# Kernel optimization log

Hardware: AMD Instinct MI355X
Metric: run time of the kernel (lower is better)

Reference implementation:

```python
import jax, jax.numpy as jnp
import numpy as np

PIECES = 64  # self.plane


def _proj(f, w1, b1, w2, b2):
    # Projection: fc2(relu(fc1(f))), final_relu=False
    h = jax.nn.relu(f @ w1 + b1)
    return h @ w2 + b2


def _cf(img, param, pieces):
    # img: [B,3,H,W], param: [B,3,P]
    # total[b,c,h,w] = sum_i clamp(img - i/P, 0, 1/P) * param[b,c,i], then * P / sum_i param
    grid = jnp.arange(pieces, dtype=img.dtype) / pieces            # [P]
    clipped = jnp.clip(img[..., None] - grid, 0.0, 1.0 / pieces)   # [B,3,H,W,P]
    total = jnp.einsum('bchwp,bcp->bchw', clipped, param)
    norm = pieces / (jnp.sum(param, axis=-1) + 1e-30)              # [B,3]
    return total * norm[:, :, None, None]


def setup_inputs() -> dict:
    key = jax.random.key(0)
    ks = jax.random.split(key, 11)
    B, H, W = 8, 256, 256
    s = 0.05
    return {
        'x': jax.random.uniform(ks[0], (B, 3, H, W), jnp.float32),
        'f_feature': jax.random.normal(ks[1], (B, 512), jnp.float32),
        'b_feature': jax.random.normal(ks[2], (B, 512), jnp.float32),
        # stacked weights for [fc_f_1, fc_b_1, fc_f_s, fc_b_s]
        'proj_w1': jax.random.normal(ks[3], (4, 512, 192), jnp.float32) * s,
        'proj_b1': jax.random.normal(ks[4], (4, 192), jnp.float32) * s,
        'proj_w2': jax.random.normal(ks[5], (4, 192, 192), jnp.float32) * s,
        'proj_b2': jax.random.normal(ks[6], (4, 192), jnp.float32) * s,
        'fc_w1': jax.random.normal(ks[7], (576, 192), jnp.float32) * s,
        'fc_b1': jax.random.normal(ks[8], (192,), jnp.float32) * s,
        'fc_w2': jax.random.normal(ks[9], (192, 192), jnp.float32) * s,
        'fc_b2': jax.random.normal(ks[10], (192,), jnp.float32) * s,
    }


def reference(x, f_feature, b_feature, proj_w1, proj_b1, proj_w2, proj_b2,
              fc_w1, fc_b1, fc_w2, fc_b2):
    B = x.shape[0]
    # rgb_to_grayscale with 3 output channels (ITU-R 601 weights)
    gw = jnp.array([0.299, 0.587, 0.114], dtype=x.dtype)
    gray = jnp.broadcast_to(jnp.einsum('bchw,c->bhw', x, gw)[:, None], x.shape)

    # four stacked Projections: inputs [f, b, f, b]
    feats = jnp.stack([f_feature, b_feature, f_feature, b_feature])       # [4,B,512]
    h = jax.nn.relu(jnp.einsum('kbi,kio->kbo', feats, proj_w1) + proj_b1[:, None, :])
    outs = jnp.einsum('kbo,koq->kbq', h, proj_w2) + proj_b2[:, None, :]   # [4,B,192]
    param_f, param_b = outs[0], outs[1]
    param_s = outs[2] + outs[3]

    cat = jnp.concatenate([param_f, param_b, param_s], axis=1)            # [B,576]
    param = _proj(cat, fc_w1, fc_b1, fc_w2, fc_b2)                        # [B,192]

    p_all = param.reshape(B, 3, PIECES)
    p_f = param_f.reshape(B, 3, PIECES)
    p_b = param_b.reshape(B, 3, PIECES)

    return (_cf(x, p_all, PIECES), _cf(gray, p_f, PIECES), _cf(gray, p_b, PIECES))
```

## Files before the change

### kernel.cpp

```cpp
#include <hip/hip_runtime.h>

#define HWSZ 65536
#define PLANE (3 * HWSZ)
#define OUTSTRIDE (8 * PLANE)
#define MAGIC 0x13572468

__global__ __launch_bounds__(384) void k_mlp(
    const float* __restrict__ f, const float* __restrict__ bf,
    const float* __restrict__ pw1, const float* __restrict__ pb1,
    const float* __restrict__ pw2, const float* __restrict__ pb2,
    const float* __restrict__ fw1, const float* __restrict__ fb1,
    const float* __restrict__ fw2, const float* __restrict__ fb2,
    float* __restrict__ ws) {
  __shared__ float smem[2304];
  int t = threadIdx.x, blk = blockIdx.x;

  float* pA      = ws;
  float* partial = ws + 12288;
  int* fbase = (int*)(ws + 20480);

  int s = blk & 7, b = blk >> 3;
  int k = s >> 1, half = s & 1, o0 = half * 96;
  {
    float* sf  = smem;
    float* red = smem + 512;
    float* sh  = smem + 2048;

    const float* feat = ((k & 1) ? bf : f) + b * 512;
    for (int i = t; i < 512; i += 384) sf[i] = feat[i];
    __syncthreads();

    {
      int q = t % 24, sr = t / 24;
      const float4* w = (const float4*)(pw1 + (size_t)k * (512 * 192));
      int icol = half * 24 + q;
      float4 acc = {0.f, 0.f, 0.f, 0.f};
      int i0 = sr * 32;
      for (int r = 0; r < 2; ++r) {
        float4 wv[16];
#pragma unroll
        for (int j = 0; j < 16; ++j)
          wv[j] = w[(size_t)(i0 + r * 16 + j) * 48 + icol];
#pragma unroll
        for (int j = 0; j < 16; ++j) {
          float v = sf[i0 + r * 16 + j];
          acc.x = fmaf(v, wv[j].x, acc.x); acc.y = fmaf(v, wv[j].y, acc.y);
          acc.z = fmaf(v, wv[j].z, acc.z); acc.w = fmaf(v, wv[j].w, acc.w);
        }
      }
      ((float4*)(red + sr * 96))[q] = acc;
    }
    __syncthreads();
    if (t < 96) {
      float a = pb1[k * 192 + o0 + t];
#pragma unroll
      for (int s2 = 0; s2 < 16; ++s2) a += red[s2 * 96 + t];
      sh[t] = fmaxf(a, 0.f);
    }
    __syncthreads();
    {
      int q2 = t % 48, s2 = t / 48;
      const float4* w = (const float4*)(pw2 + (size_t)k * (192 * 192));
      float4 acc = {0.f, 0.f, 0.f, 0.f};
      float4 wv[12];
#pragma unroll
      for (int j = 0; j < 12; ++j)
        wv[j] = w[(size_t)(o0 + s2 * 12 + j) * 48 + q2];
#pragma unroll
      for (int j = 0; j < 12; ++j) {
        float v = sh[s2 * 12 + j];
        acc.x = fmaf(v, wv[j].x, acc.x); acc.y = fmaf(v, wv[j].y, acc.y);
        acc.z = fmaf(v, wv[j].z, acc.z); acc.w = fmaf(v, wv[j].w, acc.w);
      }
      ((float4*)(red + s2 * 192))[q2] = acc;
    }
    __syncthreads();
    if (t < 192) {
      float a = 0.f;
#pragma unroll
      for (int s3 = 0; s3 < 8; ++s3) a += red[s3 * 192 + t];
      pA[((k * 8 + b) * 2 + half) * 192 + t] = a;
    }
    __syncthreads();
    if (t == 0) {
      __threadfence();
      atomicExch(&fbase[blk * 16], MAGIC);
    }
  }

  if (s >= 4) return;

  int b2 = b, c4 = s, ob2 = c4 * 48;
  int q = t % 12, sb = t / 12;
  int q2 = t % 48, s2 = t / 48;

  float4 wv1[18];
  {
    const float4* w = (const float4*)fw1;
    int i0 = sb * 18;
#pragma unroll
    for (int j = 0; j < 18; ++j)
      wv1[j] = w[(size_t)(i0 + j) * 48 + c4 * 12 + q];
  }
  float4 wv2[6];
  {
    const float4* w = (const float4*)fw2;
#pragma unroll
    for (int j = 0; j < 6; ++j)
      wv2[j] = w[(size_t)(ob2 + s2 * 6 + j) * 48 + q2];
  }

  if (t < 8) {
    while (atomicAdd(&fbase[((b2 << 3) + t) * 16], 0) != MAGIC)
      __builtin_amdgcn_s_sleep(2);
  }
  __syncthreads();
  if (t == 0) __threadfence();
  __syncthreads();

  {
    float* sc  = smem;
    float* red = smem + 576;
    for (int idx = t; idx < 576; idx += 384) {
      float v;
      if (idx < 192) {
        const float* p0 = pA + ((0 * 8 + b2) * 2) * 192;
        v = p0[idx] + p0[192 + idx] + pb2[idx];
      } else if (idx < 384) {
        int jj = idx - 192;
        const float* p1 = pA + ((1 * 8 + b2) * 2) * 192;
        v = p1[jj] + p1[192 + jj] + pb2[192 + jj];
      } else {
        int jj = idx - 384;
        const float* p2 = pA + ((2 * 8 + b2) * 2) * 192;
        const float* p3 = pA + ((3 * 8 + b2) * 2) * 192;
        v = p2[jj] + p2[192 + jj] + p3[jj] + p3[192 + jj] +
            pb2[384 + jj] + pb2[576 + jj];
      }
      sc[idx] = v;
    }
    __syncthreads();
    {
      float4 acc = {0.f, 0.f, 0.f, 0.f};
      int i0 = sb * 18;
#pragma unroll
      for (int j = 0; j < 18; ++j) {
        float v = sc[i0 + j];
        acc.x = fmaf(v, wv1[j].x, acc.x); acc.y = fmaf(v, wv1[j].y, acc.y);
        acc.z = fmaf(v, wv1[j].z, acc.z); acc.w = fmaf(v, wv1[j].w, acc.w);
      }
      ((float4*)(red + sb * 48))[q] = acc;
    }
    __syncthreads();
    if (t < 48) {
      float a = fb1[ob2 + t];
#pragma unroll
      for (int s3 = 0; s3 < 32; ++s3) a += red[s3 * 48 + t];
      smem[t] = fmaxf(a, 0.f);
    }
    __syncthreads();
    {
      float4 acc = {0.f, 0.f, 0.f, 0.f};
#pragma unroll
      for (int j = 0; j < 6; ++j) {
        float v = smem[s2 * 6 + j];
        acc.x = fmaf(v, wv2[j].x, acc.x); acc.y = fmaf(v, wv2[j].y, acc.y);
        acc.z = fmaf(v, wv2[j].z, acc.z); acc.w = fmaf(v, wv2[j].w, acc.w);
      }
      ((float4*)(red + s2 * 192))[q2] = acc;
    }
    __syncthreads();
    if (t < 192) {
      float a = (c4 == 0) ? fb2[t] : 0.f;
#pragma unroll
      for (int s3 = 0; s3 < 8; ++s3) a += red[s3 * 192 + t];
      partial[(c4 * 8 + b2) * 192 + t] = a;
    }
  }
}

__global__ __launch_bounds__(256) void k_render(
    const float* __restrict__ x, const float* __restrict__ ws,
    const float* __restrict__ pb2, float* __restrict__ out) {
  int b = blockIdx.y, t = threadIdx.x;
  int wave = t >> 6, lane = t & 63;
  const float* pA      = ws;
  const float* partial = ws + 12288;
  __shared__ float2 tab[576];

  int s4a = blockIdx.x * 512 + t, s4b = s4a + 256;
  const float* xb = x + (size_t)b * PLANE;
  float4 vr0 = ((const float4*)(xb))[s4a];
  float4 vr1 = ((const float4*)(xb))[s4b];
  float4 vg0 = ((const float4*)(xb + HWSZ))[s4a];
  float4 vg1 = ((const float4*)(xb + HWSZ))[s4b];
  float4 vb0 = ((const float4*)(xb + 2 * HWSZ))[s4a];
  float4 vb1 = ((const float4*)(xb + 2 * HWSZ))[s4b];

  for (int cur = wave; cur < 9; cur += 4) {
    int oi = cur / 3, c = cur - oi * 3;
    float p;
    if (oi == 0) {
      const float* pp = partial + b * 192 + c * 64;
      p = pp[lane] + pp[1536 + lane] + pp[3072 + lane] + pp[4608 + lane];
    } else {
      const float* pa = pA + (((oi - 1) * 8 + b) * 2) * 192 + c * 64;
      p = pa[lane] + pa[192 + lane] + pb2[(oi - 1) * 192 + c * 64 + lane];
    }
    float v = p;
#pragma unroll
    for (int d = 1; d < 64; d <<= 1) {
      float n = __shfl_up(v, d, 64);
      if (lane >= d) v += n;
    }
    float total = __shfl(v, 63, 64);
    float norm = 64.f / (total + 1e-30f);
    tab[cur * 64 + lane] = make_float2((v - p) * 0.015625f * norm, p * norm);
  }
  __syncthreads();

  auto idx_of = [&](float v, int& kk, float& tt) {
    int k = (int)(v * 64.f);
    k = k < 0 ? 0 : (k > 63 ? 63 : k);
    kk = k;
    tt = v - (float)k * 0.015625f;
  };
  auto evk = [&](int cur, int k, float tt) -> float {
    float2 e = tab[cur * 64 + k];
    return fmaf(tt, e.y, e.x);
  };
  auto ev4 = [&](int cur, float4 v) -> float4 {
    int k; float tt; float4 r;
    idx_of(v.x, k, tt); r.x = evk(cur, k, tt);
    idx_of(v.y, k, tt); r.y = evk(cur, k, tt);
    idx_of(v.z, k, tt); r.z = evk(cur, k, tt);
    idx_of(v.w, k, tt); r.w = evk(cur, k, tt);
    return r;
  };

  float* o0 = out + (size_t)b * PLANE;
  float* o1 = out + OUTSTRIDE + (size_t)b * PLANE;
  float* o2 = out + 2 * OUTSTRIDE + (size_t)b * PLANE;

  auto process = [&](int s4, float4 vr, float4 vg, float4 vb) {
    float4 gr;
    gr.x = fmaf(0.299f, vr.x, fmaf(0.587f, vg.x, 0.114f * vb.x));
    gr.y = fmaf(0.299f, vr.y, fmaf(0.587f, vg.y, 0.114f * vb.y));
    gr.z = fmaf(0.299f, vr.z, fmaf(0.587f, vg.z, 0.114f * vb.z));
    gr.w = fmaf(0.299f, vr.w, fmaf(0.587f, vg.w, 0.114f * vb.w));

    ((float4*)(o0))[s4]            = ev4(0, vr);
    ((float4*)(o0 + HWSZ))[s4]     = ev4(1, vg);
    ((float4*)(o0 + 2 * HWSZ))[s4] = ev4(2, vb);

    int kx, ky, kz, kw; float tx, ty, tz, tw;
    idx_of(gr.x, kx, tx); idx_of(gr.y, ky, ty);
    idx_of(gr.z, kz, tz); idx_of(gr.w, kw, tw);
#pragma unroll
    for (int c = 0; c < 3; ++c) {
      float4 r;
      r.x = evk(3 + c, kx, tx); r.y = evk(3 + c, ky, ty);
      r.z = evk(3 + c, kz, tz); r.w = evk(3 + c, kw, tw);
      ((float4*)(o1 + c * HWSZ))[s4] = r;
    }
#pragma unroll
    for (int c = 0; c < 3; ++c) {
      float4 r;
      r.x = evk(6 + c, kx, tx); r.y = evk(6 + c, ky, ty);
      r.z = evk(6 + c, kz, tz); r.w = evk(6 + c, kw, tw);
      ((float4*)(o2 + c * HWSZ))[s4] = r;
    }
  };

  process(s4a, vr0, vg0, vb0);
  process(s4b, vr1, vg1, vb1);
}

extern "C" void kernel_launch(void* const* d_in, const int* in_sizes, int n_in,
                              void* d_out, int out_size, void* d_ws, size_t ws_size,
                              hipStream_t stream) {
  const float* x   = (const float*)d_in[0];
  const float* f   = (const float*)d_in[1];
  const float* bf  = (const float*)d_in[2];
  const float* pw1 = (const float*)d_in[3];
  const float* pb1 = (const float*)d_in[4];
  const float* pw2 = (const float*)d_in[5];
  const float* pb2 = (const float*)d_in[6];
  const float* fw1 = (const float*)d_in[7];
  const float* fb1 = (const float*)d_in[8];
  const float* fw2 = (const float*)d_in[9];
  const float* fb2 = (const float*)d_in[10];
  float* out = (float*)d_out;
  float* ws  = (float*)d_ws;

  k_mlp<<<64, 384, 0, stream>>>(f, bf, pw1, pb1, pw2, pb2, fw1, fb1, fw2,
                                fb2, ws);
  dim3 grid(32, 8);
  k_render<<<grid, 256, 0, stream>>>(x, ws, pb2, out);
}
```

Baseline: 94.44 us.

## Fuse MLP and render into one kernel with flag-based stage overlap

New measurement: 103.0 us. 9.1% more time.

```diff
diff --git a/kernel.cpp b/kernel.cpp
--- a/kernel.cpp
+++ b/kernel.cpp
@@ -5,208 +5,221 @@
 #define OUTSTRIDE (8 * PLANE)
 #define MAGIC 0x13572468
 
-__global__ __launch_bounds__(384) void k_mlp(
+__device__ __forceinline__ void waitflag(const int* p) {
+  while (__hip_atomic_load(p, __ATOMIC_RELAXED, __HIP_MEMORY_SCOPE_AGENT) !=
+         MAGIC)
+    __builtin_amdgcn_s_sleep(4);
+}
+
+__global__ __launch_bounds__(512) void k_fused(
+    const float* __restrict__ x,
     const float* __restrict__ f, const float* __restrict__ bf,
     const float* __restrict__ pw1, const float* __restrict__ pb1,
     const float* __restrict__ pw2, const float* __restrict__ pb2,
     const float* __restrict__ fw1, const float* __restrict__ fb1,
     const float* __restrict__ fw2, const float* __restrict__ fb2,
-    float* __restrict__ ws) {
+    float* __restrict__ ws, float* __restrict__ out) {
   __shared__ float smem[2304];
-  int t = threadIdx.x, blk = blockIdx.x;
+  __shared__ float2 tab[576];
+  const int t = threadIdx.x, bid = blockIdx.x;
 
   float* pA      = ws;
   float* partial = ws + 12288;
   int* fbase = (int*)(ws + 20480);
 
-  int s = blk & 7, b = blk >> 3;
-  int k = s >> 1, half = s & 1, o0 = half * 96;
-  {
-    float* sf  = smem;
-    float* red = smem + 512;
-    float* sh  = smem + 2048;
-
-    const float* feat = ((k & 1) ? bf : f) + b * 512;
-    for (int i = t; i < 512; i += 384) sf[i] = feat[i];
-    __syncthreads();
+  const int bx = bid >> 3, b_r = bid & 7;
+  const int s4 = bx * 512 + t;
+  const float* xb = x + (size_t)b_r * PLANE;
+  float4 vr, vg, vb;
+
+  const bool is_mlp = (bid < 64);
+  if (!is_mlp) {
+    vr = ((const float4*)(xb))[s4];
+    vg = ((const float4*)(xb + HWSZ))[s4];
+    vb = ((const float4*)(xb + 2 * HWSZ))[s4];
+    asm volatile("" :: "v"(vr.x), "v"(vg.x), "v"(vb.x));
+  }
+
+  if (is_mlp) {
+    const int s = bid & 7, b = bid >> 3;
+    const int k = s >> 1, half = s & 1, o0c = half * 96;
 
     {
-      int q = t % 24, sr = t / 24;
-      const float4* w = (const float4*)(pw1 + (size_t)k * (512 * 192));
-      int icol = half * 24 + q;
-      float4 acc = {0.f, 0.f, 0.f, 0.f};
-      int i0 = sr * 32;
-      for (int r = 0; r < 2; ++r) {
-        float4 wv[16];
-#pragma unroll
-        for (int j = 0; j < 16; ++j)
-          wv[j] = w[(size_t)(i0 + r * 16 + j) * 48 + icol];
-#pragma unroll
-        for (int j = 0; j < 16; ++j) {
-          float v = sf[i0 + r * 16 + j];
+      float* sf  = smem;
+      float* red = smem + 512;
+      float* sh  = smem + 2048;
+
+      const float* feat = ((k & 1) ? bf : f) + b * 512;
+      sf[t] = feat[t & 511];
+      __syncthreads();
+
+      if (t < 384) {
+        int q = t % 24, sr = t / 24;
+        const float4* w = (const float4*)(pw1 + (size_t)k * (512 * 192));
+        int icol = half * 24 + q;
+        float4 acc = {0.f, 0.f, 0.f, 0.f};
+        int i0 = sr * 32;
+        for (int r = 0; r < 2; ++r) {
+          float4 wv[16];
+#pragma unroll
+          for (int j = 0; j < 16; ++j)
+            wv[j] = w[(size_t)(i0 + r * 16 + j) * 48 + icol];
+#pragma unroll
+          for (int j = 0; j < 16; ++j) {
+            float v = sf[i0 + r * 16 + j];
+            acc.x = fmaf(v, wv[j].x, acc.x); acc.y = fmaf(v, wv[j].y, acc.y);
+            acc.z = fmaf(v, wv[j].z, acc.z); acc.w = fmaf(v, wv[j].w, acc.w);
+          }
+        }
+        ((float4*)(red + sr * 96))[q] = acc;
+      }
+      __syncthreads();
+      if (t < 96) {
+        float a = pb1[k * 192 + o0c + t];
+#pragma unroll
+        for (int s2 = 0; s2 < 16; ++s2) a += red[s2 * 96 + t];
+        sh[t] = fmaxf(a, 0.f);
+      }
+      __syncthreads();
+      if (t < 384) {
+        int q2 = t % 48, s2 = t / 48;
+        const float4* w = (const float4*)(pw2 + (size_t)k * (192 * 192));
+        float4 acc = {0.f, 0.f, 0.f, 0.f};
+        float4 wv[12];
+#pragma unroll
+        for (int j = 0; j < 12; ++j)
+          wv[j] = w[(size_t)(o0c + s2 * 12 + j) * 48 + q2];
+#pragma unroll
+        for (int j = 0; j < 12; ++j) {
+          float v = sh[s2 * 12 + j];
           acc.x = fmaf(v, wv[j].x, acc.x); acc.y = fmaf(v, wv[j].y, acc.y);
           acc.z = fmaf(v, wv[j].z, acc.z); acc.w = fmaf(v, wv[j].w, acc.w);
         }
-      }
-      ((float4*)(red + sr * 96))[q] = acc;
-    }
-    __syncthreads();
-    if (t < 96) {
-      float a = pb1[k * 192 + o0 + t];
-#pragma unroll
-      for (int s2 = 0; s2 < 16; ++s2) a += red[s2 * 96 + t];
-      sh[t] = fmaxf(a, 0.f);
-    }
-    __syncthreads();
-    {
+        ((float4*)(red + s2 * 192))[q2] = acc;
+      }
+      __syncthreads();
+      if (t < 192) {
+        float a = 0.f;
+#pragma unroll
+        for (int s3 = 0; s3 < 8; ++s3) a += red[s3 * 192 + t];
+        pA[((k * 8 + b) * 2 + half) * 192 + t] = a;
+      }
+      __syncthreads();
+      if (t == 0) {
+        __threadfence();
+        atomicExch(&fbase[bid * 32], MAGIC);
+      }
+    }
+
+    if (s < 4) {
+      const int b2 = b, c4 = s, ob2 = c4 * 48;
+      int q = t % 12, sb = t / 12;
       int q2 = t % 48, s2 = t / 48;
-      const float4* w = (const float4*)(pw2 + (size_t)k * (192 * 192));
-      float4 acc = {0.f, 0.f, 0.f, 0.f};
-      float4 wv[12];
-#pragma unroll
-      for (int j = 0; j < 12; ++j)
-        wv[j] = w[(size_t)(o0 + s2 * 12 + j) * 48 + q2];
-#pragma unroll
-      for (int j = 0; j < 12; ++j) {
-        float v = sh[s2 * 12 + j];
-        acc.x = fmaf(v, wv[j].x, acc.x); acc.y = fmaf(v, wv[j].y, acc.y);
-        acc.z = fmaf(v, wv[j].z, acc.z); acc.w = fmaf(v, wv[j].w, acc.w);
-      }
-      ((float4*)(red + s2 * 192))[q2] = acc;
-    }
-    __syncthreads();
-    if (t < 192) {
-      float a = 0.f;
-#pragma unroll
-      for (int s3 = 0; s3 < 8; ++s3) a += red[s3 * 192 + t];
-      pA[((k * 8 + b) * 2 + half) * 192 + t] = a;
-    }
-    __syncthreads();
-    if (t == 0) {
-      __threadfence();
-      atomicExch(&fbase[blk * 16], MAGIC);
-    }
-  }
-
-  if (s >= 4) return;
-
-  int b2 = b, c4 = s, ob2 = c4 * 48;
-  int q = t % 12, sb = t / 12;
-  int q2 = t % 48, s2 = t / 48;
-
-  float4 wv1[18];
-  {
-    const float4* w = (const float4*)fw1;
-    int i0 = sb * 18;
-#pragma unroll
-    for (int j = 0; j < 18; ++j)
-      wv1[j] = w[(size_t)(i0 + j) * 48 + c4 * 12 + q];
-  }
-  float4 wv2[6];
-  {
-    const float4* w = (const float4*)fw2;
-#pragma unroll
-    for (int j = 0; j < 6; ++j)
-      wv2[j] = w[(size_t)(ob2 + s2 * 6 + j) * 48 + q2];
-  }
-
-  if (t < 8) {
-    while (atomicAdd(&fbase[((b2 << 3) + t) * 16], 0) != MAGIC)
-      __builtin_amdgcn_s_sleep(2);
-  }
+
+      float4 wv1[18];
+      if (t < 384) {
+        const float4* w = (const float4*)fw1;
+        int i0 = sb * 18;
+#pragma unroll
+        for (int j = 0; j < 18; ++j)
+          wv1[j] = w[(size_t)(i0 + j) * 48 + c4 * 12 + q];
+      }
+      float4 wv2[6];
+      if (t < 384) {
+        const float4* w = (const float4*)fw2;
+#pragma unroll
+        for (int j = 0; j < 6; ++j)
+          wv2[j] = w[(size_t)(ob2 + s2 * 6 + j) * 48 + q2];
+      }
+
+      if (t < 8) waitflag(&fbase[((b2 << 3) + t) * 32]);
+      __syncthreads();
+      if (t == 0) __threadfence();
+      __syncthreads();
+
+      {
+        float* sc  = smem;
+        float* red = smem + 576;
+        for (int idx = t; idx < 576; idx += 512) {
+          float v;
+          if (idx < 192) {
+            const float* p0 = pA + ((0 * 8 + b2) * 2) * 192;
+            v = p0[idx] + p0[192 + idx] + pb2[idx];
+          } else if (idx < 384) {
+            int jj = idx - 192;
+            const float* p1 = pA + ((1 * 8 + b2) * 2) * 192;
+            v = p1[jj] + p1[192 + jj] + pb2[192 + jj];
+          } else {
+            int jj = idx - 384;
+            const float* p2 = pA + ((2 * 8 + b2) * 2) * 192;
+            const float* p3 = pA + ((3 * 8 + b2) * 2) * 192;
+            v = p2[jj] + p2[192 + jj] + p3[jj] + p3[192 + jj] +
+                pb2[384 + jj] + pb2[576 + jj];
+          }
+          sc[idx] = v;
+        }
+        __syncthreads();
+        if (t < 384) {
+          float4 acc = {0.f, 0.f, 0.f, 0.f};
+          int i0 = sb * 18;
+#pragma unroll
+          for (int j = 0; j < 18; ++j) {
+            float v = sc[i0 + j];
+            acc.x = fmaf(v, wv1[j].x, acc.x); acc.y = fmaf(v, wv1[j].y, acc.y);
+            acc.z = fmaf(v, wv1[j].z, acc.z); acc.w = fmaf(v, wv1[j].w, acc.w);
+          }
+          ((float4*)(red + sb * 48))[q] = acc;
+        }
+        __syncthreads();
+        if (t < 48) {
+          float a = fb1[ob2 + t];
+#pragma unroll
+          for (int s3 = 0; s3 < 32; ++s3) a += red[s3 * 48 + t];
+          smem[t] = fmaxf(a, 0.f);
+        }
+        __syncthreads();
+        if (t < 384) {
+          float4 acc = {0.f, 0.f, 0.f, 0.f};
+#pragma unroll
+          for (int j = 0; j < 6; ++j) {
+            float v = smem[s2 * 6 + j];
+            acc.x = fmaf(v, wv2[j].x, acc.x); acc.y = fmaf(v, wv2[j].y, acc.y);
+            acc.z = fmaf(v, wv2[j].z, acc.z); acc.w = fmaf(v, wv2[j].w, acc.w);
+          }
+          ((float4*)(red + s2 * 192))[q2] = acc;
+        }
+        __syncthreads();
+        if (t < 192) {
+          float a = (c4 == 0) ? fb2[t] : 0.f;
+#pragma unroll
+          for (int s3 = 0; s3 < 8; ++s3) a += red[s3 * 192 + t];
+          partial[(c4 * 8 + b2) * 192 + t] = a;
+        }
+        __syncthreads();
+        if (t == 0) {
+          __threadfence();
+          atomicExch(&fbase[(64 + c4 * 8 + b2) * 32], MAGIC);
+        }
+      }
+    }
+
+    vr = ((const float4*)(xb))[s4];
+    vg = ((const float4*)(xb + HWSZ))[s4];
+    vb = ((const float4*)(xb + 2 * HWSZ))[s4];
+  }
+
+  if (t < 4) waitflag(&fbase[(b_r * 8 + t) * 32]);
   __syncthreads();
   if (t == 0) __threadfence();
   __syncthreads();
 
-  {
-    float* sc  = smem;
-    float* red = smem + 576;
-    for (int idx = t; idx < 576; idx += 384) {
-      float v;
-      if (idx < 192) {
-        const float* p0 = pA + ((0 * 8 + b2) * 2) * 192;
-        v = p0[idx] + p0[192 + idx] + pb2[idx];
-      } else if (idx < 384) {
-        int jj = idx - 192;
-        const float* p1 = pA + ((1 * 8 + b2) * 2) * 192;
-        v = p1[jj] + p1[192 + jj] + pb2[192 + jj];
-      } else {
-        int jj = idx - 384;
-        const float* p2 = pA + ((2 * 8 + b2) * 2) * 192;
-        const float* p3 = pA + ((3 * 8 + b2) * 2) * 192;
-        v = p2[jj] + p2[192 + jj] + p3[jj] + p3[192 + jj] +
-            pb2[384 + jj] + pb2[576 + jj];
-      }
-      sc[idx] = v;
-    }
-    __syncthreads();
-    {
-      float4 acc = {0.f, 0.f, 0.f, 0.f};
-      int i0 = sb * 18;
-#pragma unroll
-      for (int j = 0; j < 18; ++j) {
-        float v = sc[i0 + j];
-        acc.x = fmaf(v, wv1[j].x, acc.x); acc.y = fmaf(v, wv1[j].y, acc.y);
-        acc.z = fmaf(v, wv1[j].z, acc.z); acc.w = fmaf(v, wv1[j].w, acc.w);
-      }
-      ((float4*)(red + sb * 48))[q] = acc;
-    }
-    __syncthreads();
-    if (t < 48) {
-      float a = fb1[ob2 + t];
-#pragma unroll
-      for (int s3 = 0; s3 < 32; ++s3) a += red[s3 * 48 + t];
-      smem[t] = fmaxf(a, 0.f);
-    }
-    __syncthreads();
-    {
-      float4 acc = {0.f, 0.f, 0.f, 0.f};
-#pragma unroll
-      for (int j = 0; j < 6; ++j) {
-        float v = smem[s2 * 6 + j];
-        acc.x = fmaf(v, wv2[j].x, acc.x); acc.y = fmaf(v, wv2[j].y, acc.y);
-        acc.z = fmaf(v, wv2[j].z, acc.z); acc.w = fmaf(v, wv2[j].w, acc.w);
-      }
-      ((float4*)(red + s2 * 192))[q2] = acc;
-    }
-    __syncthreads();
-    if (t < 192) {
-      float a = (c4 == 0) ? fb2[t] : 0.f;
-#pragma unroll
-      for (int s3 = 0; s3 < 8; ++s3) a += red[s3 * 192 + t];
-      partial[(c4 * 8 + b2) * 192 + t] = a;
-    }
-  }
-}
-
-__global__ __launch_bounds__(256) void k_render(
-    const float* __restrict__ x, const float* __restrict__ ws,
-    const float* __restrict__ pb2, float* __restrict__ out) {
-  int b = blockIdx.y, t = threadIdx.x;
-  int wave = t >> 6, lane = t & 63;
-  const float* pA      = ws;
-  const float* partial = ws + 12288;
-  __shared__ float2 tab[576];
-
-  int s4a = blockIdx.x * 512 + t, s4b = s4a + 256;
-  const float* xb = x + (size_t)b * PLANE;
-  float4 vr0 = ((const float4*)(xb))[s4a];
-  float4 vr1 = ((const float4*)(xb))[s4b];
-  float4 vg0 = ((const float4*)(xb + HWSZ))[s4a];
-  float4 vg1 = ((const float4*)(xb + HWSZ))[s4b];
-  float4 vb0 = ((const float4*)(xb + 2 * HWSZ))[s4a];
-  float4 vb1 = ((const float4*)(xb + 2 * HWSZ))[s4b];
-
-  for (int cur = wave; cur < 9; cur += 4) {
+  const int wave = t >> 6, lane = t & 63;
+  if (wave < 6) {
+    int cur = 3 + wave;
     int oi = cur / 3, c = cur - oi * 3;
-    float p;
-    if (oi == 0) {
-      const float* pp = partial + b * 192 + c * 64;
-      p = pp[lane] + pp[1536 + lane] + pp[3072 + lane] + pp[4608 + lane];
-    } else {
-      const float* pa = pA + (((oi - 1) * 8 + b) * 2) * 192 + c * 64;
-      p = pa[lane] + pa[192 + lane] + pb2[(oi - 1) * 192 + c * 64 + lane];
-    }
+    const float* pa = pA + (((oi - 1) * 8 + b_r) * 2) * 192 + c * 64;
+    float p = pa[lane] + pa[192 + lane] +
+              pb2[(oi - 1) * 192 + c * 64 + lane];
     float v = p;
 #pragma unroll
     for (int d = 1; d < 64; d <<= 1) {
@@ -220,39 +233,27 @@
   __syncthreads();
 
   auto idx_of = [&](float v, int& kk, float& tt) {
-    int k = (int)(v * 64.f);
-    k = k < 0 ? 0 : (k > 63 ? 63 : k);
-    kk = k;
-    tt = v - (float)k * 0.015625f;
+    int k2 = (int)(v * 64.f);
+    k2 = k2 < 0 ? 0 : (k2 > 63 ? 63 : k2);
+    kk = k2;
+    tt = v - (float)k2 * 0.015625f;
   };
-  auto evk = [&](int cur, int k, float tt) -> float {
-    float2 e = tab[cur * 64 + k];
+  auto evk = [&](int cur, int k2, float tt) -> float {
+    float2 e = tab[cur * 64 + k2];
     return fmaf(tt, e.y, e.x);
   };
-  auto ev4 = [&](int cur, float4 v) -> float4 {
-    int k; float tt; float4 r;
-    idx_of(v.x, k, tt); r.x = evk(cur, k, tt);
-    idx_of(v.y, k, tt); r.y = evk(cur, k, tt);
-    idx_of(v.z, k, tt); r.z = evk(cur, k, tt);
-    idx_of(v.w, k, tt); r.w = evk(cur, k, tt);
-    return r;
-  };
-
-  float* o0 = out + (size_t)b * PLANE;
-  float* o1 = out + OUTSTRIDE + (size_t)b * PLANE;
-  float* o2 = out + 2 * OUTSTRIDE + (size_t)b * PLANE;
-
-  auto process = [&](int s4, float4 vr, float4 vg, float4 vb) {
+
+  float* o0 = out + (size_t)b_r * PLANE;
+  float* o1 = out + OUTSTRIDE + (size_t)b_r * PLANE;
+  float* o2 = out + 2 * OUTSTRIDE + (size_t)b_r * PLANE;
+
+  {
     float4 gr;
     gr.x = fmaf(0.299f, vr.x, fmaf(0.587f, vg.x, 0.114f * vb.x));
     gr.y = fmaf(0.299f, vr.y, fmaf(0.587f, vg.y, 0.114f * vb.y));
     gr.z = fmaf(0.299f, vr.z, fmaf(0.587f, vg.z, 0.114f * vb.z));
     gr.w = fmaf(0.299f, vr.w, fmaf(0.587f, vg.w, 0.114f * vb.w));
 
-    ((float4*)(o0))[s4]            = ev4(0, vr);
-    ((float4*)(o0 + HWSZ))[s4]     = ev4(1, vg);
-    ((float4*)(o0 + 2 * HWSZ))[s4] = ev4(2, vb);
-
     int kx, ky, kz, kw; float tx, ty, tz, tw;
     idx_of(gr.x, kx, tx); idx_of(gr.y, ky, ty);
     idx_of(gr.z, kz, tz); idx_of(gr.w, kw, tw);
@@ -270,10 +271,41 @@
       r.z = evk(6 + c, kz, tz); r.w = evk(6 + c, kw, tw);
       ((float4*)(o2 + c * HWSZ))[s4] = r;
     }
-  };
-
-  process(s4a, vr0, vg0, vb0);
-  process(s4b, vr1, vg1, vb1);
+  }
+
+  if (t < 4) waitflag(&fbase[(64 + t * 8 + b_r) * 32]);
+  __syncthreads();
+  if (t == 0) __threadfence();
+  __syncthreads();
+
+  if (wave < 3) {
+    const float* pp = partial + b_r * 192 + wave * 64;
+    float p = pp[lane] + pp[1536 + lane] + pp[3072 + lane] + pp[4608 + lane];
+    float v = p;
+#pragma unroll
+    for (int d = 1; d < 64; d <<= 1) {
+      float n = __shfl_up(v, d, 64);
+      if (lane >= d) v += n;
+    }
+    float total = __shfl(v, 63, 64);
+    float norm = 64.f / (total + 1e-30f);
+    tab[wave * 64 + lane] = make_float2((v - p) * 0.015625f * norm, p * norm);
+  }
+  __syncthreads();
+
+  {
+    auto ev4 = [&](int cur, float4 v4) -> float4 {
+      int k2; float tt; float4 r;
+      idx_of(v4.x, k2, tt); r.x = evk(cur, k2, tt);
+      idx_of(v4.y, k2, tt); r.y = evk(cur, k2, tt);
+      idx_of(v4.z, k2, tt); r.z = evk(cur, k2, tt);
+      idx_of(v4.w, k2, tt); r.w = evk(cur, k2, tt);
+      return r;
+    };
+    ((float4*)(o0))[s4]            = ev4(0, vr);
+    ((float4*)(o0 + HWSZ))[s4]     = ev4(1, vg);
+    ((float4*)(o0 + 2 * HWSZ))[s4] = ev4(2, vb);
+  }
 }
 
 extern "C" void kernel_launch(void* const* d_in, const int* in_sizes, int n_in,
@@ -293,8 +325,6 @@
   float* out = (float*)d_out;
   float* ws  = (float*)d_ws;
 
-  k_mlp<<<64, 384, 0, stream>>>(f, bf, pw1, pb1, pw2, pb2, fw1, fb1, fw2,
-                                fb2, ws);
-  dim3 grid(32, 8);
-  k_render<<<grid, 256, 0, stream>>>(x, ws, pb2, out);
+  k_fused<<<256, 512, 0, stream>>>(x, f, bf, pw1, pb1, pw2, pb2,
+                                   fw1, fb1, fw2, fb2, ws, out);
 }
```
